# Performance work log

Measured on AMD Instinct MI355X. Metric: run time of the kernel, lower is better.

Reference implementation:

```python
import jax, jax.numpy as jnp
import numpy as np

D_MODEL = 2048
N_HEADS = 16
GKV = 4
D_FF = 8192
D_HEAD = D_MODEL // N_HEADS
EPS = 1e-6


def rmsnorm(x, w):
    ms = jnp.mean(x * x, axis=-1, keepdims=True)
    return x * jax.lax.rsqrt(ms + EPS) * w


def attention(q, k, v, mask=None):
    # q: (B,Tq,H,d), k/v: (B,Tk,H,d)
    scale = 1.0 / jnp.sqrt(jnp.asarray(q.shape[-1], q.dtype))
    scores = jnp.einsum('bqhd,bkhd->bhqk', q, k) * scale
    if mask is not None:
        scores = scores + mask
    probs = jax.nn.softmax(scores, axis=-1)
    return jnp.einsum('bhqk,bkhd->bqhd', probs, v)


def setup_inputs() -> dict:
    key = jax.random.key(0)
    ks = jax.random.split(key, 12)
    B, T = 2, 2048
    s = 0.02
    return {
        'x': jax.random.normal(ks[0], (B, T, D_MODEL), jnp.float32),
        'k_ctx': jax.random.normal(ks[1], (B, T, GKV, D_HEAD), jnp.float32),
        'v_ctx': jax.random.normal(ks[2], (B, T, GKV, D_HEAD), jnp.float32),
        # cross-attn params (weights stored as (in, out); y = x @ W)
        'wq': jax.random.normal(ks[3], (D_MODEL, D_MODEL), jnp.float32) * s,
        'wo_cross': jax.random.normal(ks[4], (D_MODEL, D_MODEL), jnp.float32) * s,
        'norm_q_w': jnp.ones((D_MODEL,), jnp.float32),
        # self-attn params
        'wqkv': jax.random.normal(ks[5], (D_MODEL, 3 * D_MODEL), jnp.float32) * s,
        'wo_self': jax.random.normal(ks[6], (D_MODEL, D_MODEL), jnp.float32) * s,
        'norm_qkv_w': jnp.ones((D_MODEL,), jnp.float32),
        # FFN params (bias=False in FeedForward)
        'ffn_w1': jax.random.normal(ks[7], (D_MODEL, D_FF), jnp.float32) * s,
        'ffn_w2': jax.random.normal(ks[8], (D_FF, D_MODEL), jnp.float32) * s,
        'ffn_norm_w': jnp.ones((D_MODEL,), jnp.float32),
    }


def reference(x, k_ctx, v_ctx, wq, wo_cross, norm_q_w, wqkv, wo_self,
              norm_qkv_w, ffn_w1, ffn_w2, ffn_norm_w):
    B, T, D = x.shape
    repeat = N_HEADS // GKV

    # ---- cross attention (GQA) ----
    q = (rmsnorm(x, norm_q_w) @ wq).reshape(B, T, N_HEADS, D_HEAD)
    k = jnp.repeat(k_ctx, repeat, axis=2)  # (B,Tk,H,d), matches repeat_interleave
    v = jnp.repeat(v_ctx, repeat, axis=2)
    ctx = attention(q, k, v, mask=None).reshape(B, T, D)
    x = x + ctx @ wo_cross

    # ---- causal self attention ----
    xn = rmsnorm(x, norm_qkv_w)
    qkv = xn @ wqkv
    qs, ks_, vs = jnp.split(qkv, 3, axis=-1)
    qs = qs.reshape(B, T, N_HEADS, D_HEAD)
    ks_ = ks_.reshape(B, T, N_HEADS, D_HEAD)
    vs = vs.reshape(B, T, N_HEADS, D_HEAD)
    causal_mask = jnp.triu(jnp.full((T, T), -jnp.inf, x.dtype), k=1)[None, None]
    ctx2 = attention(qs, ks_, vs, mask=causal_mask).reshape(B, T, D)
    x = x + ctx2 @ wo_self

    # ---- FFN (SiLU) ----
    h = rmsnorm(x, ffn_norm_w)
    y = jax.nn.silu(h @ ffn_w1) @ ffn_w2
    return x + y
```

## Files before the change

kernel.cpp:

```cpp
#include <hip/hip_runtime.h>
#include <math.h>

typedef unsigned short u16;
typedef __attribute__((ext_vector_type(4))) u16 u16x4;
typedef __attribute__((ext_vector_type(8))) u16 u16x8;
typedef __attribute__((ext_vector_type(8))) __bf16 bf16x8;
typedef __attribute__((ext_vector_type(4))) float f32x4;
typedef __attribute__((ext_vector_type(16))) float f32x16;
typedef __attribute__((ext_vector_type(4))) unsigned u32x4;

#define D_MODEL 2048
#define SEQ 2048
#define BATCH 2
#define NH 16
#define HD 128
#define DFF 8192
#define ROWS (BATCH * SEQ)

__device__ __forceinline__ u16 f2bf(float f) {
  union { float f; unsigned u; } v; v.f = f;
  unsigned r = v.u + 0x7FFFu + ((v.u >> 16) & 1u);
  return (u16)(r >> 16);
}
__device__ __forceinline__ u16 to_bf16(float f) { return f2bf(f); }
__device__ __forceinline__ u16 to_bf16(u16 v) { return v; }

__device__ __forceinline__ f32x4 mfma16(u16x8 a, u16x8 b, f32x4 c) {
  return __builtin_amdgcn_mfma_f32_16x16x32_bf16(
      __builtin_bit_cast(bf16x8, a), __builtin_bit_cast(bf16x8, b), c, 0, 0, 0);
}
__device__ __forceinline__ f32x16 mfma32(u16x8 a, u16x8 b, f32x16 c) {
  return __builtin_amdgcn_mfma_f32_32x32x16_bf16(
      __builtin_bit_cast(bf16x8, a), __builtin_bit_cast(bf16x8, b), c, 0, 0, 0);
}

__device__ __forceinline__ void gll16(const void* g, void* l) {
  __builtin_amdgcn_global_load_lds(
      (const __attribute__((address_space(1))) void*)g,
      (__attribute__((address_space(3))) void*)l, 16, 0, 0);
}

__global__ __launch_bounds__(256) void cast_kernel(const float* __restrict__ in,
                                                   u16* __restrict__ out, int n8) {
  int i = blockIdx.x * 256 + threadIdx.x;
  if (i >= n8) return;
  const float4* p = (const float4*)in + (size_t)i * 2;
  float4 a = p[0], b = p[1];
  u16x8 o;
  o[0] = f2bf(a.x); o[1] = f2bf(a.y); o[2] = f2bf(a.z); o[3] = f2bf(a.w);
  o[4] = f2bf(b.x); o[5] = f2bf(b.y); o[6] = f2bf(b.z); o[7] = f2bf(b.w);
  *((u16x8*)out + i) = o;
}

__global__ __launch_bounds__(256) void cast_transpose_kernel(
    const float* __restrict__ in, u16* __restrict__ out, int K, int N) {
  __shared__ float tile[64][65];
  int n0 = blockIdx.x * 64, k0 = blockIdx.y * 64;
  int tx = threadIdx.x & 63, ty = threadIdx.x >> 6;
#pragma unroll
  for (int i = 0; i < 64; i += 4)
    tile[ty + i][tx] = in[(size_t)(k0 + ty + i) * N + n0 + tx];
  __syncthreads();
#pragma unroll
  for (int i = 0; i < 64; i += 4)
    out[(size_t)(n0 + ty + i) * K + k0 + tx] = f2bf(tile[tx][ty + i]);
}

template <typename ST>
__global__ __launch_bounds__(256) void build_vt_kernel(
    const ST* __restrict__ src, u16* __restrict__ dst, int HZ,
    size_t src_b_stride, size_t src_h_stride, int src_tok_stride) {
  __shared__ u16 tl[64][72];
  int z = blockIdx.z, zb = z / HZ, zh = z % HZ;
  const ST* s = src + (size_t)zb * src_b_stride + (size_t)zh * src_h_stride;
  int t0 = blockIdx.x * 64, d0 = blockIdx.y * 64;
  int rr = threadIdx.x >> 4, cc = (threadIdx.x & 15) * 4;
#pragma unroll
  for (int pp = 0; pp < 4; ++pp) {
    int t = pp * 16 + rr;
    const ST* sp = s + (size_t)(t0 + t) * src_tok_stride + d0 + cc;
#pragma unroll
    for (int j = 0; j < 4; ++j) tl[t][cc + j] = to_bf16(sp[j]);
  }
  __syncthreads();
  u16* dp = dst + (size_t)z * HD * SEQ;
#pragma unroll
  for (int pp = 0; pp < 4; ++pp) {
    int d = pp * 16 + rr;
    u16x4 w;
#pragma unroll
    for (int j = 0; j < 4; ++j) w[j] = tl[cc + j][d];
    *(u16x4*)(dp + (size_t)(d0 + d) * SEQ + t0 + cc) = w;
  }
}

__global__ __launch_bounds__(256) void rmsnorm_kernel(const float* __restrict__ x,
                                                      const float* __restrict__ w,
                                                      u16* __restrict__ out) {
  __shared__ float red[4];
  int row = blockIdx.x, t = threadIdx.x;
  const float4* xr = (const float4*)(x + (size_t)row * D_MODEL);
  float4 a = xr[t * 2], b = xr[t * 2 + 1];
  float ss = a.x * a.x + a.y * a.y + a.z * a.z + a.w * a.w +
             b.x * b.x + b.y * b.y + b.z * b.z + b.w * b.w;
#pragma unroll
  for (int m = 1; m < 64; m <<= 1) ss += __shfl_xor(ss, m, 64);
  if ((t & 63) == 0) red[t >> 6] = ss;
  __syncthreads();
  float tot = red[0] + red[1] + red[2] + red[3];
  float sc = rsqrtf(tot * (1.0f / D_MODEL) + 1e-6f);
  const float4* wr = (const float4*)w;
  float4 wa = wr[t * 2], wb = wr[t * 2 + 1];
  u16x8 o;
  o[0] = f2bf(a.x * sc * wa.x); o[1] = f2bf(a.y * sc * wa.y);
  o[2] = f2bf(a.z * sc * wa.z); o[3] = f2bf(a.w * sc * wa.w);
  o[4] = f2bf(b.x * sc * wb.x); o[5] = f2bf(b.y * sc * wb.y);
  o[6] = f2bf(b.z * sc * wb.z); o[7] = f2bf(b.w * sc * wb.w);
  *((u16x8*)(out + (size_t)row * D_MODEL) + t) = o;
}

template <int MODE>
__global__ __launch_bounds__(256) void combine_kernel(
    const float* __restrict__ p0, const float* __restrict__ p1,
    const float* __restrict__ res, void* __restrict__ outv, int n4) {
  int i = blockIdx.x * 256 + threadIdx.x;
  if (i >= n4) return;
  float4 a = ((const float4*)p0)[i];
  float4 b = ((const float4*)p1)[i];
  if (MODE == 1) {
    float4 r = ((const float4*)res)[i];
    float4 o;
    o.x = r.x + a.x + b.x; o.y = r.y + a.y + b.y;
    o.z = r.z + a.z + b.z; o.w = r.w + a.w + b.w;
    ((float4*)outv)[i] = o;
  } else {
    u16x4 o;
    o[0] = f2bf(a.x + b.x); o[1] = f2bf(a.y + b.y);
    o[2] = f2bf(a.z + b.z); o[3] = f2bf(a.w + b.w);
    ((u16x4*)outv)[i] = o;
  }
}

#define GPHASE(T, P, VM, ISSUE)                                                \
  {                                                                            \
    if (ISSUE) issue_half(4 * (T) + (P) + 4);                                  \
    asm volatile("s_waitcnt vmcnt(" #VM ")" ::: "memory");                     \
    __builtin_amdgcn_sched_barrier(0);                                         \
    __builtin_amdgcn_s_barrier();                                              \
    if (((P) & 1) == 0) {                                                      \
      const u16* SA = S + (((((T) & 1) << 2) | (((P) >> 1) << 1)) << 13);      \
      const u16* SB = SA + 8192;                                               \
      _Pragma("unroll") for (int m = 0; m < 8; ++m) {                          \
        int row = wm * 128 + m * 16 + r16;                                     \
        aF[m] = *(const u16x8*)(SA + row * 32 + ((kg ^ ((row >> 1) & 3)) << 3)); \
      }                                                                        \
      _Pragma("unroll") for (int n = 0; n < 4; ++n) {                          \
        int row = wn * 64 + n * 16 + r16;                                      \
        bF[n] = *(const u16x8*)(SB + row * 32 + ((kg ^ ((row >> 1) & 3)) << 3)); \
      }                                                                        \
    }                                                                          \
    __builtin_amdgcn_s_setprio(1);                                             \
    _Pragma("unroll") for (int m = 0; m < 8; ++m) {                            \
      acc[m][2 * ((P) & 1)] = mfma16(aF[m], bF[2 * ((P) & 1)], acc[m][2 * ((P) & 1)]); \
      acc[m][2 * ((P) & 1) + 1] =                                              \
          mfma16(aF[m], bF[2 * ((P) & 1) + 1], acc[m][2 * ((P) & 1) + 1]);     \
    }                                                                          \
    __builtin_amdgcn_s_setprio(0);                                             \
    __builtin_amdgcn_s_barrier();                                              \
  }

template <int EPI, int SPLIT>
__global__ __launch_bounds__(512, 1) void gemm256_kernel(
    const u16* __restrict__ A, const u16* __restrict__ Bt, void* __restrict__ Cv,
    float* __restrict__ Cv2, const float* __restrict__ res, int N, int K) {
  __shared__ __align__(16) u16 S[8 * 8192];
  const int tid = threadIdx.x, lane = tid & 63, wave = tid >> 6;
  const int wm = wave >> 2, wn = wave & 3;
  const int r16 = lane & 15, kg = lane >> 4;
  const int cols = N >> 8;
  const int cpx = gridDim.x >> 3;
  const int bid = blockIdx.x;
  const int swz = (bid & 7) * cpx + (bid >> 3);
  const int tiles = gridDim.x / SPLIT;
  const int tile = swz % tiles, kslice = swz / tiles;
  const int bm = (tile / cols) * 256, bn = (tile % cols) * 256;
  const int Ksub = K / SPLIT;
  const int koff = kslice * Ksub;
  const int nt = Ksub >> 6;

  auto issue_half = [&](int h) {
    int p = h & 3, t = h >> 2;
    const u16* src = (p & 1) ? (Bt + (size_t)bn * K) : (A + (size_t)bm * K);
    int kbase = koff + t * 64 + (p >> 1) * 32;
    u16* ldst = S + ((((t & 1) << 2) | p) << 13);
#pragma unroll
    for (int i = 0; i < 2; ++i) {
      int c = i * 512 + tid;
      int row = c >> 2, ch = c & 3;
      int kc = ch ^ ((row >> 1) & 3);
      gll16(src + (size_t)row * K + kbase + kc * 8, ldst + c * 8);
    }
  };

  u16x8 aF[8], bF[4];
  f32x4 acc[8][4] = {};

  issue_half(0); issue_half(1); issue_half(2); issue_half(3);
  for (int t = 0; t < nt - 1; ++t) {
    GPHASE(t, 0, 6, true);
    GPHASE(t, 1, 6, true);
    GPHASE(t, 2, 6, true);
    GPHASE(t, 3, 6, true);
  }
  {
    const int t = nt - 1;
    GPHASE(t, 0, 4, false);
    GPHASE(t, 1, 4, false);
    GPHASE(t, 2, 0, false);
    GPHASE(t, 3, 0, false);
  }

  float* Pp = (EPI == 3) ? (kslice ? Cv2 : (float*)Cv) : nullptr;
#pragma unroll
  for (int m = 0; m < 8; ++m) {
    int r0 = bm + wm * 128 + m * 16 + kg * 4;
#pragma unroll
    for (int n = 0; n < 4; ++n) {
      int cc = bn + wn * 64 + n * 16 + r16;
#pragma unroll
      for (int r = 0; r < 4; ++r) {
        size_t idx = (size_t)(r0 + r) * N + cc;
        float v = acc[m][n][r];
        if (EPI == 3) {
          Pp[idx] = v;
        } else if (EPI == 1) {
          ((float*)Cv)[idx] = res[idx] + v;
        } else if (EPI == 0) {
          ((u16*)Cv)[idx] = f2bf(v);
        } else {
          float s = v / (1.0f + __expf(-v));
          ((u16*)Cv)[idx] = f2bf(s);
        }
      }
    }
  }
}

template <bool CAUSAL, bool SELF>
__global__ __launch_bounds__(512, 2) void attn2_kernel(
    const u16* __restrict__ qp, const u16* __restrict__ kp,
    const u16* __restrict__ vtp, u16* __restrict__ outp) {
  __shared__ __align__(16) u16 Kl[64 * 128];
  __shared__ __align__(16) u16 Vl[128 * 64];
  const int tid = threadIdx.x, lane = tid & 63, wave = tid >> 6;
  const int lo = lane & 31, hi = lane >> 5;
  const int qt = blockIdx.x, bh = blockIdx.y, b = bh >> 4, h = bh & 15;
  const int qw0 = qt * 256 + wave * 32;
  const int qg = qw0 + lo;
  const size_t qstr = SELF ? 6144 : 2048;
  const size_t kstr = SELF ? 6144 : 512;
  const u16* qbase = qp + ((size_t)b * SEQ + qg) * qstr + h * HD;
  const u16* kbase = kp + (size_t)b * SEQ * kstr + (SELF ? (2048 + h * HD) : ((h >> 2) * HD));
  const u16* vbase = vtp + (size_t)(SELF ? (b * NH + h) : (b * 4 + (h >> 2))) * HD * SEQ;

  u16x8 qf[8];
#pragma unroll
  for (int dc = 0; dc < 8; ++dc) qf[dc] = *(const u16x8*)(qbase + dc * 16 + hi * 8);

  f32x16 o[4] = {};
  float m_run = -3e38f, l_run = 0.f;
  const int ntiles = CAUSAL ? qt * 4 + 4 : SEQ / 64;
  const float scale = 0.088388347648318447f;

  for (int kt = 0; kt < ntiles; ++kt) {
    __syncthreads();
#pragma unroll
    for (int i = 0; i < 2; ++i) {
      int c = i * 512 + tid;
      int krow = c >> 4, ks = c & 15;
      gll16(kbase + (size_t)(kt * 64 + krow) * kstr + ((ks ^ (krow & 15)) * 8),
            Kl + (size_t)c * 8);
      int vd = c >> 3, vs = c & 7;
      gll16(vbase + (size_t)vd * SEQ + kt * 64 + ((vs ^ (vd & 7)) * 8),
            Vl + (size_t)c * 8);
    }
    __syncthreads();
    if (CAUSAL && kt * 64 > qw0 + 31) continue;

    f32x16 s01[2] = {};
#pragma unroll
    for (int k2 = 0; k2 < 2; ++k2) {
      int key = k2 * 32 + lo;
#pragma unroll
      for (int mf = 0; mf < 8; ++mf) {
        int dc = mf * 2 + hi;
        u16x8 kf = *(const u16x8*)(Kl + key * 128 + ((dc ^ (key & 15)) * 8));
        s01[k2] = mfma32(kf, qf[mf], s01[k2]);
      }
    }

    float sv[32];
    float pm = -3e38f;
#pragma unroll
    for (int k2 = 0; k2 < 2; ++k2)
#pragma unroll
      for (int r = 0; r < 16; ++r) {
        float v = s01[k2][r];
        if (CAUSAL) {
          int key = kt * 64 + k2 * 32 + (r & 3) + 8 * (r >> 2) + 4 * hi;
          if (key > qg) v = -3e38f;
        }
        sv[k2 * 16 + r] = v;
        pm = fmaxf(pm, v);
      }
    pm = fmaxf(pm, __shfl_xor(pm, 32, 64));
    float mn = fmaxf(m_run, pm);
    float corr = __expf((m_run - mn) * scale);
    m_run = mn;

    float ps = 0.f;
    u16x8 pf[4];
#pragma unroll
    for (int k2 = 0; k2 < 2; ++k2)
#pragma unroll
      for (int hf = 0; hf < 2; ++hf) {
        float p8[8];
#pragma unroll
        for (int j = 0; j < 8; ++j) {
          p8[j] = __expf((sv[k2 * 16 + hf * 8 + j] - mn) * scale);
          ps += p8[j];
        }
        unsigned w0, w1, w2, w3;
        asm("v_cvt_pk_bf16_f32 %0, %1, %2" : "=v"(w0) : "v"(p8[0]), "v"(p8[1]));
        asm("v_cvt_pk_bf16_f32 %0, %1, %2" : "=v"(w1) : "v"(p8[2]), "v"(p8[3]));
        asm("v_cvt_pk_bf16_f32 %0, %1, %2" : "=v"(w2) : "v"(p8[4]), "v"(p8[5]));
        asm("v_cvt_pk_bf16_f32 %0, %1, %2" : "=v"(w3) : "v"(p8[6]), "v"(p8[7]));
        asm("v_permlane32_swap_b32 %0, %1" : "+v"(w0), "+v"(w2));
        asm("v_permlane32_swap_b32 %0, %1" : "+v"(w1), "+v"(w3));
        u32x4 fr; fr[0] = w0; fr[1] = w1; fr[2] = w2; fr[3] = w3;
        pf[k2 * 2 + hf] = __builtin_bit_cast(u16x8, fr);
      }
    ps += __shfl_xor(ps, 32, 64);
    l_run = l_run * corr + ps;

#pragma unroll
    for (int mb = 0; mb < 4; ++mb)
#pragma unroll
      for (int r = 0; r < 16; ++r) o[mb][r] *= corr;

#pragma unroll
    for (int kc = 0; kc < 4; ++kc) {
      int vcs = kc * 2 + hi;
#pragma unroll
      for (int mb = 0; mb < 4; ++mb) {
        int d = mb * 32 + lo;
        u16x8 vf = *(const u16x8*)(Vl + d * 64 + ((vcs ^ (d & 7)) * 8));
        o[mb] = mfma32(vf, pf[kc], o[mb]);
      }
    }
  }

  float inv = 1.0f / l_run;
  u16* ob = outp + ((size_t)b * SEQ + qg) * D_MODEL + h * HD + 4 * hi;
#pragma unroll
  for (int mb = 0; mb < 4; ++mb)
#pragma unroll
    for (int rq = 0; rq < 4; ++rq) {
      u16x4 w;
#pragma unroll
      for (int j = 0; j < 4; ++j) w[j] = f2bf(o[mb][rq * 4 + j] * inv);
      *(u16x4*)(ob + mb * 32 + rq * 8) = w;
    }
}

extern "C" void kernel_launch(void* const* d_in, const int* in_sizes, int n_in,
                              void* d_out, int out_size, void* d_ws, size_t ws_size,
                              hipStream_t stream) {
  const float* x          = (const float*)d_in[0];
  const float* k_ctx      = (const float*)d_in[1];
  const float* v_ctx      = (const float*)d_in[2];
  const float* wq         = (const float*)d_in[3];
  const float* wo_cross   = (const float*)d_in[4];
  const float* norm_q_w   = (const float*)d_in[5];
  const float* wqkv       = (const float*)d_in[6];
  const float* wo_self    = (const float*)d_in[7];
  const float* norm_qkv_w = (const float*)d_in[8];
  const float* ffn_w1     = (const float*)d_in[9];
  const float* ffn_w2     = (const float*)d_in[10];
  const float* ffn_norm_w = (const float*)d_in[11];
  float* out = (float*)d_out;

  char* ws = (char*)d_ws;
  size_t off = 0;
  auto alloc_u16 = [&](size_t n) { u16* p = (u16*)(ws + off); off += n * 2; return p; };
  auto alloc_f32 = [&](size_t n) { float* p = (float*)(ws + off); off += n * 4; return p; };
  u16* wq_bf   = alloc_u16((size_t)2048 * 2048);
  u16* woc_bf  = alloc_u16((size_t)2048 * 2048);
  u16* wqkv_bf = alloc_u16((size_t)2048 * 6144);
  u16* wos_bf  = alloc_u16((size_t)2048 * 2048);
  u16* w1_bf   = alloc_u16((size_t)2048 * 8192);
  u16* w2_bf   = alloc_u16((size_t)8192 * 2048);
  u16* xn_bf   = alloc_u16((size_t)ROWS * 2048);
  u16* qkv_bf  = alloc_u16((size_t)ROWS * 6144);
  u16* attn_bf = alloc_u16((size_t)ROWS * 2048);
  float* x1    = alloc_f32((size_t)ROWS * 2048);
  float* x2    = alloc_f32((size_t)ROWS * 2048);
  u16* q_bf    = qkv_bf;
  u16* h1_bf   = qkv_bf;
  u16* kc_bf   = (u16*)x2;
  u16* vt_ctx  = kc_bf + (size_t)BATCH * SEQ * 4 * HD;
  u16* vt_self = xn_bf;
  float* Pq1  = (float*)((char*)qkv_bf + 16777216);
  float* Pqkv = (float*)qkv_bf;
  const int n4 = ROWS * 2048 / 4;

  auto castT = [&](const float* src, u16* dst, int K, int N) {
    cast_transpose_kernel<<<dim3(N / 64, K / 64), 256, 0, stream>>>(src, dst, K, N);
  };
  castT(wq, wq_bf, 2048, 2048);
  castT(wo_cross, woc_bf, 2048, 2048);
  castT(wqkv, wqkv_bf, 2048, 6144);
  castT(wo_self, wos_bf, 2048, 2048);
  castT(ffn_w1, w1_bf, 2048, 8192);
  castT(ffn_w2, w2_bf, 8192, 2048);
  {
    int n8 = (int)((size_t)BATCH * SEQ * 4 * HD / 8);
    cast_kernel<<<dim3((n8 + 255) / 256), dim3(256), 0, stream>>>(k_ctx, kc_bf, n8);
  }
  build_vt_kernel<float><<<dim3(SEQ / 64, HD / 64, BATCH * 4), 256, 0, stream>>>(
      v_ctx, vt_ctx, 4, (size_t)SEQ * 512, (size_t)HD, 512);

  rmsnorm_kernel<<<ROWS, 256, 0, stream>>>(x, norm_q_w, xn_bf);
  gemm256_kernel<3, 2><<<dim3(256), 512, 0, stream>>>(
      xn_bf, wq_bf, x1, Pq1, nullptr, 2048, 2048);
  combine_kernel<0><<<dim3((n4 + 255) / 256), 256, 0, stream>>>(
      x1, Pq1, nullptr, q_bf, n4);
  attn2_kernel<false, false><<<dim3(SEQ / 256, BATCH * NH), 512, 0, stream>>>(
      q_bf, kc_bf, vt_ctx, attn_bf);
  gemm256_kernel<3, 2><<<dim3(256), 512, 0, stream>>>(
      attn_bf, woc_bf, x1, Pqkv, nullptr, 2048, 2048);
  combine_kernel<1><<<dim3((n4 + 255) / 256), 256, 0, stream>>>(
      x1, Pqkv, x, x1, n4);

  rmsnorm_kernel<<<ROWS, 256, 0, stream>>>(x1, norm_qkv_w, xn_bf);
  gemm256_kernel<0, 1><<<dim3((ROWS / 256) * (6144 / 256)), 512, 0, stream>>>(
      xn_bf, wqkv_bf, qkv_bf, nullptr, nullptr, 6144, 2048);
  build_vt_kernel<u16><<<dim3(SEQ / 64, HD / 64, BATCH * NH), 256, 0, stream>>>(
      qkv_bf + 4096, vt_self, NH, (size_t)SEQ * 6144, (size_t)HD, 6144);
  attn2_kernel<true, true><<<dim3(SEQ / 256, BATCH * NH), 512, 0, stream>>>(
      qkv_bf, qkv_bf, vt_self, attn_bf);
  gemm256_kernel<3, 2><<<dim3(256), 512, 0, stream>>>(
      attn_bf, wos_bf, x2, Pqkv, nullptr, 2048, 2048);
  combine_kernel<1><<<dim3((n4 + 255) / 256), 256, 0, stream>>>(
      x2, Pqkv, x1, x2, n4);

  rmsnorm_kernel<<<ROWS, 256, 0, stream>>>(x2, ffn_norm_w, xn_bf);
  gemm256_kernel<2, 1><<<dim3((ROWS / 256) * (8192 / 256)), 512, 0, stream>>>(
      xn_bf, w1_bf, h1_bf, nullptr, nullptr, 8192, 2048);
  gemm256_kernel<3, 2><<<dim3(256), 512, 0, stream>>>(
      h1_bf, w2_bf, out, x1, nullptr, 2048, 8192);
  combine_kernel<1><<<dim3((n4 + 255) / 256), 256, 0, stream>>>(
      out, x1, x2, out, n4);
}
```

Measured before the change: 878.4 us.

## Add 256x128-tile GEMM kernel replacing split-K GEMMs plus combine passes

Adds a new GEMM kernel with 256x128 output tiles, 16x16 MFMA, an XOR-swizzled LDS layout and a four-stage global-to-LDS async pipeline. It replaces the split-K 256x256 GEMM plus separate combine kernel for the square projections, and the 256x256 GEMM for the QKV projection. Smaller tiles give 256 blocks for N=2048 without split-K, which removes the fp32 partial buffer round-trip and the extra combine launches. The cost is lower per-block reuse and different MFMA shapes.

```diff
diff --git a/kernel.cpp b/kernel.cpp
--- a/kernel.cpp
+++ b/kernel.cpp
@@ -246,6 +246,100 @@
   }
 }
 
+#define NPHASE(T, P, VM, ISSUE)                                                \
+  {                                                                            \
+    if (ISSUE) issue_pair(2 * (T) + (P) + 2);                                  \
+    asm volatile("s_waitcnt vmcnt(" #VM ")" ::: "memory");                     \
+    __builtin_amdgcn_sched_barrier(0);                                         \
+    __builtin_amdgcn_s_barrier();                                              \
+    const u16* SA = S + ((((T) & 1) * 2 + (P)) * 12288);                       \
+    const u16* SB = SA + 8192;                                                 \
+    u16x8 aF[4], bF[4];                                                        \
+    _Pragma("unroll") for (int m = 0; m < 4; ++m) {                            \
+      int row = wm * 64 + m * 16 + r16;                                        \
+      aF[m] = *(const u16x8*)(SA + row * 32 + ((kg ^ ((row >> 1) & 3)) << 3)); \
+    }                                                                          \
+    _Pragma("unroll") for (int n = 0; n < 4; ++n) {                            \
+      int row = wn * 64 + n * 16 + r16;                                        \
+      bF[n] = *(const u16x8*)(SB + row * 32 + ((kg ^ ((row >> 1) & 3)) << 3)); \
+    }                                                                          \
+    __builtin_amdgcn_s_setprio(1);                                             \
+    _Pragma("unroll") for (int m = 0; m < 4; ++m)                              \
+      _Pragma("unroll") for (int n = 0; n < 4; ++n)                            \
+        acc[m][n] = mfma16(aF[m], bF[n], acc[m][n]);                           \
+    __builtin_amdgcn_s_setprio(0);                                             \
+    __builtin_amdgcn_s_barrier();                                              \
+  }
+
+template <int EPI>
+__global__ __launch_bounds__(512, 1) void gemm_n128_kernel(
+    const u16* __restrict__ A, const u16* __restrict__ Bt, void* __restrict__ Cv,
+    const float* __restrict__ res, int N, int K) {
+  __shared__ __align__(16) u16 S[4 * 12288];
+  const int tid = threadIdx.x, lane = tid & 63, wave = tid >> 6;
+  const int wm = wave >> 1, wn = wave & 1;
+  const int r16 = lane & 15, kg = lane >> 4;
+  const int cols = N >> 7;
+  const int cpx = gridDim.x >> 3;
+  const int bid = blockIdx.x;
+  const int swz = (bid & 7) * cpx + (bid >> 3);
+  const int bm = (swz / cols) * 256, bn = (swz % cols) * 128;
+  const int nt = K >> 6;
+
+  auto issue_pair = [&](int g) {
+    int p = g & 1, t = g >> 1;
+    int kbase = t * 64 + p * 32;
+    u16* reg = S + (((t & 1) * 2 + p) * 12288);
+#pragma unroll
+    for (int i = 0; i < 2; ++i) {
+      int c = i * 512 + tid;
+      int row = c >> 2, ch = c & 3;
+      int kc = ch ^ ((row >> 1) & 3);
+      gll16(A + (size_t)(bm + row) * K + kbase + kc * 8, reg + c * 8);
+    }
+    {
+      int row = tid >> 2, ch = tid & 3;
+      int kc = ch ^ ((row >> 1) & 3);
+      gll16(Bt + (size_t)(bn + row) * K + kbase + kc * 8, reg + 8192 + tid * 8);
+    }
+  };
+
+  f32x4 acc[4][4] = {};
+
+  issue_pair(0); issue_pair(1);
+  for (int t = 0; t < nt - 1; ++t) {
+    NPHASE(t, 0, 6, true);
+    NPHASE(t, 1, 6, true);
+  }
+  {
+    const int t = nt - 1;
+    NPHASE(t, 0, 3, false);
+    NPHASE(t, 1, 0, false);
+  }
+
+#pragma unroll
+  for (int m = 0; m < 4; ++m) {
+    int r0 = bm + wm * 64 + m * 16 + kg * 4;
+#pragma unroll
+    for (int n = 0; n < 4; ++n) {
+      int cc = bn + wn * 64 + n * 16 + r16;
+#pragma unroll
+      for (int r = 0; r < 4; ++r) {
+        size_t idx = (size_t)(r0 + r) * N + cc;
+        float v = acc[m][n][r];
+        if (EPI == 1) {
+          ((float*)Cv)[idx] = res[idx] + v;
+        } else if (EPI == 0) {
+          ((u16*)Cv)[idx] = f2bf(v);
+        } else {
+          float s = v / (1.0f + __expf(-v));
+          ((u16*)Cv)[idx] = f2bf(s);
+        }
+      }
+    }
+  }
+}
+
 template <bool CAUSAL, bool SELF>
 __global__ __launch_bounds__(512, 2) void attn2_kernel(
     const u16* __restrict__ qp, const u16* __restrict__ kp,
@@ -410,8 +504,6 @@
   u16* kc_bf   = (u16*)x2;
   u16* vt_ctx  = kc_bf + (size_t)BATCH * SEQ * 4 * HD;
   u16* vt_self = xn_bf;
-  float* Pq1  = (float*)((char*)qkv_bf + 16777216);
-  float* Pqkv = (float*)qkv_bf;
   const int n4 = ROWS * 2048 / 4;
 
   auto castT = [&](const float* src, u16* dst, int K, int N) {
@@ -431,28 +523,22 @@
       v_ctx, vt_ctx, 4, (size_t)SEQ * 512, (size_t)HD, 512);
 
   rmsnorm_kernel<<<ROWS, 256, 0, stream>>>(x, norm_q_w, xn_bf);
-  gemm256_kernel<3, 2><<<dim3(256), 512, 0, stream>>>(
-      xn_bf, wq_bf, x1, Pq1, nullptr, 2048, 2048);
-  combine_kernel<0><<<dim3((n4 + 255) / 256), 256, 0, stream>>>(
-      x1, Pq1, nullptr, q_bf, n4);
+  gemm_n128_kernel<0><<<dim3((ROWS / 256) * (2048 / 128)), 512, 0, stream>>>(
+      xn_bf, wq_bf, q_bf, nullptr, 2048, 2048);
   attn2_kernel<false, false><<<dim3(SEQ / 256, BATCH * NH), 512, 0, stream>>>(
       q_bf, kc_bf, vt_ctx, attn_bf);
-  gemm256_kernel<3, 2><<<dim3(256), 512, 0, stream>>>(
-      attn_bf, woc_bf, x1, Pqkv, nullptr, 2048, 2048);
-  combine_kernel<1><<<dim3((n4 + 255) / 256), 256, 0, stream>>>(
-      x1, Pqkv, x, x1, n4);
+  gemm_n128_kernel<1><<<dim3((ROWS / 256) * (2048 / 128)), 512, 0, stream>>>(
+      attn_bf, woc_bf, x1, x, 2048, 2048);
 
   rmsnorm_kernel<<<ROWS, 256, 0, stream>>>(x1, norm_qkv_w, xn_bf);
-  gemm256_kernel<0, 1><<<dim3((ROWS / 256) * (6144 / 256)), 512, 0, stream>>>(
-      xn_bf, wqkv_bf, qkv_bf, nullptr, nullptr, 6144, 2048);
+  gemm_n128_kernel<0><<<dim3((ROWS / 256) * (6144 / 128)), 512, 0, stream>>>(
+      xn_bf, wqkv_bf, qkv_bf, nullptr, 6144, 2048);
   build_vt_kernel<u16><<<dim3(SEQ / 64, HD / 64, BATCH * NH), 256, 0, stream>>>(
       qkv_bf + 4096, vt_self, NH, (size_t)SEQ * 6144, (size_t)HD, 6144);
   attn2_kernel<true, true><<<dim3(SEQ / 256, BATCH * NH), 512, 0, stream>>>(
       qkv_bf, qkv_bf, vt_self, attn_bf);
-  gemm256_kernel<3, 2><<<dim3(256), 512, 0, stream>>>(
-      attn_bf, wos_bf, x2, Pqkv, nullptr, 2048, 2048);
-  combine_kernel<1><<<dim3((n4 + 255) / 256), 256, 0, stream>>>(
-      x2, Pqkv, x1, x2, n4);
+  gemm_n128_kernel<1><<<dim3((ROWS / 256) * (2048 / 128)), 512, 0, stream>>>(
+      attn_bf, wos_bf, x2, x1, 2048, 2048);
 
   rmsnorm_kernel<<<ROWS, 256, 0, stream>>>(x2, ffn_norm_w, xn_bf);
   gemm256_kernel<2, 1><<<dim3((ROWS / 256) * (8192 / 256)), 512, 0, stream>>>(
```

Result: faster. 838.0 us (-4.6%).
